# Optimization experiments

Hardware: AMD Instinct MI355X
Metric: run time of the kernel (lower is better)

Reference implementation:

```python
import jax, jax.numpy as jnp
import numpy as np

N_NODES = 100000


def _gcn_norm(edge_index, num_nodes):
    # PyG GCNConv default: add self-loops, symmetric normalization
    row, col = edge_index[0], edge_index[1]
    loop = jnp.arange(num_nodes, dtype=edge_index.dtype)
    row = jnp.concatenate([row, loop])
    col = jnp.concatenate([col, loop])
    ones = jnp.ones(col.shape[0], dtype=jnp.float32)
    deg = jax.ops.segment_sum(ones, col, num_segments=num_nodes)
    dinv = jnp.where(deg > 0, jax.lax.rsqrt(deg), 0.0)
    norm = dinv[row] * dinv[col]  # [E + N]
    return row, col, norm


def _gcn_conv(x, W, b, row, col, norm, num_nodes):
    h = x @ W                               # [N, out] linear transform first
    msg = h[row] * norm[:, None]            # gather + edge-wise scale
    out = jax.ops.segment_sum(msg, col, num_segments=num_nodes)  # scatter-add
    return out + b


def setup_inputs() -> dict:
    key = jax.random.key(0)
    k1, k2, k3, k4 = jax.random.split(key, 4)
    E = 1600000
    x = jax.random.normal(k1, (N_NODES, 128), dtype=jnp.float32)
    edge_index = jax.random.randint(k2, (2, E), 0, N_NODES, dtype=jnp.int64)
    W1 = jax.random.normal(k3, (128, 128), dtype=jnp.float32) * (1.0 / np.sqrt(128))
    b1 = jnp.zeros((128,), dtype=jnp.float32)
    W2 = jax.random.normal(k4, (128, 64), dtype=jnp.float32) * (1.0 / np.sqrt(128))
    b2 = jnp.zeros((64,), dtype=jnp.float32)
    return {"x": x, "edge_index": edge_index, "W1": W1, "b1": b1, "W2": W2, "b2": b2}


def reference(x, edge_index, W1, b1, W2, b2):
    num_nodes = x.shape[0]
    row, col, norm = _gcn_norm(edge_index, num_nodes)
    h = _gcn_conv(x, W1, b1, row, col, norm, num_nodes)
    h = jax.nn.relu(h)
    out = _gcn_conv(h, W2, b2, row, col, norm, num_nodes)
    return out
```

## Files before the change

kernel.cpp:

```cpp
#include <hip/hip_runtime.h>
#include <hip/hip_bf16.h>

typedef unsigned short u16;
typedef unsigned char u8;
typedef short bf16x8 __attribute__((ext_vector_type(8)));
typedef float f32x4 __attribute__((ext_vector_type(4)));

__device__ __forceinline__ float bflo(unsigned u) { return __uint_as_float(u << 16); }
__device__ __forceinline__ float bfhi(unsigned u) { return __uint_as_float(u & 0xffff0000u); }
__device__ __forceinline__ u16 f2bf(float f) {
    unsigned u = __float_as_uint(f);
    return (u16)((u + 0x7fffu + ((u >> 16) & 1u)) >> 16);
}

#define CHUNK 8192
#define BN 512

#define PK_RMASK 0x7fffffu

__global__ __launch_bounds__(256) void hist_prep_kernel(const int* __restrict__ cols,
                                                        unsigned* __restrict__ hist,
                                                        int E, int nbuckets, int nblocksA,
                                                        const float* __restrict__ W1,
                                                        const float* __restrict__ W2,
                                                        u16* __restrict__ WT1,
                                                        u16* __restrict__ WT2) {
    int blk = blockIdx.x;
    if (blk >= nblocksA) {
        int t = (blk - nblocksA) * 256 + threadIdx.x;
        if (t < 128 * 128) {
            int n = t >> 7, k = t & 127;
            WT1[n * 128 + k] = f2bf(W1[k * 128 + n]);
        } else if (t < 128 * 128 + 64 * 128) {
            int i = t - 128 * 128;
            int n = i >> 7, k = i & 127;
            WT2[n * 128 + k] = f2bf(W2[k * 64 + n]);
        }
        return;
    }
    __shared__ unsigned h[256];
    int t = threadIdx.x;
    h[t] = 0;
    __syncthreads();
    int base = blk * CHUNK;
#pragma unroll
    for (int j = 0; j < CHUNK / 256; j++) {
        int i = base + j * 256 + t;
        if (i < E) atomicAdd(&h[((unsigned)cols[i]) >> 9], 1u);
    }
    __syncthreads();
    if (t < nbuckets) hist[blk * nbuckets + t] = h[t];
}

__global__ __launch_bounds__(256) void scanA1_kernel(unsigned* __restrict__ hist,
                                                     unsigned* __restrict__ totals,
                                                     int nblocksA, int nbuckets) {
    __shared__ unsigned s[256];
    int t = threadIdx.x, b = blockIdx.x;
    unsigned val = (t < nblocksA) ? hist[t * nbuckets + b] : 0u;
    s[t] = val;
    __syncthreads();
    for (int off = 1; off < 256; off <<= 1) {
        unsigned v = (t >= off) ? s[t - off] : 0u;
        __syncthreads();
        s[t] += v;
        __syncthreads();
    }
    if (t < nblocksA) hist[t * nbuckets + b] = s[t] - val;
    if (t == 255) totals[b] = s[255];
}

__global__ __launch_bounds__(256) void scanA2_kernel(const unsigned* __restrict__ totals,
                                                     unsigned* __restrict__ bucketbase,
                                                     int nbuckets) {
    __shared__ unsigned s[256];
    int t = threadIdx.x;
    unsigned val = (t < nbuckets) ? totals[t] : 0u;
    s[t] = val;
    __syncthreads();
    for (int off = 1; off < 256; off <<= 1) {
        unsigned v = (t >= off) ? s[t - off] : 0u;
        __syncthreads();
        s[t] += v;
        __syncthreads();
    }
    unsigned ex = s[t] - val;
    if (t < nbuckets) bucketbase[t] = ex;
    if (t == nbuckets - 1) bucketbase[nbuckets] = ex + val;
}

__global__ __launch_bounds__(256) void scatterA_kernel(const int* __restrict__ rows,
                                                       const int* __restrict__ cols,
                                                       const unsigned* __restrict__ hist,
                                                       const unsigned* __restrict__ bucketbase,
                                                       unsigned* __restrict__ binned,
                                                       int E, int nbuckets) {
    __shared__ unsigned sp[CHUNK];
    __shared__ u8 spg[CHUNK];
    __shared__ unsigned lstart[256];
    __shared__ unsigned lcur[256];
    __shared__ unsigned gbase[256];
    int t = threadIdx.x, blk = blockIdx.x;
    int base = blk * CHUNK;
    int cnt = min(CHUNK, E - base);

    lcur[t] = 0;
    __syncthreads();
    for (int i = t; i < cnt; i += 256)
        atomicAdd(&lcur[((unsigned)cols[base + i]) >> 9], 1u);
    __syncthreads();
    unsigned val = lcur[t];
    lstart[t] = val;
    __syncthreads();
    for (int off = 1; off < 256; off <<= 1) {
        unsigned v = (t >= off) ? lstart[t - off] : 0u;
        __syncthreads();
        lstart[t] += v;
        __syncthreads();
    }
    unsigned ex = lstart[t] - val;
    __syncthreads();
    lstart[t] = ex;
    lcur[t] = ex;
    if (t < nbuckets) gbase[t] = bucketbase[t] + hist[blk * nbuckets + t];
    __syncthreads();
    for (int i = t; i < cnt; i += 256) {
        unsigned c = (unsigned)cols[base + i];
        unsigned r = (unsigned)rows[base + i];
        unsigned g = c >> 9;
        unsigned pos = atomicAdd(&lcur[g], 1u);
        sp[pos] = r | ((c & 511u) << 23);
        spg[pos] = (u8)g;
    }
    __syncthreads();
    for (int i = t; i < cnt; i += 256) {
        unsigned pk = sp[i];
        unsigned g = spg[i];
        binned[gbase[g] + (unsigned)i - lstart[g]] = pk;
    }
}

__global__ __launch_bounds__(256) void binB_kernel(const unsigned* __restrict__ binned,
                                                   const unsigned* __restrict__ bucketbase,
                                                   int* __restrict__ rowptr,
                                                   float* __restrict__ dinv,
                                                   int* __restrict__ srcidx,
                                                   int N, int E, int nbuckets) {
    __shared__ unsigned cnt[BN + 1];
    __shared__ unsigned sc[BN + 1];
    __shared__ unsigned ps[256];
    int t = threadIdx.x, b = blockIdx.x;
    int lo = b << 9;
    int nn = min(BN, N - lo);
    unsigned s = bucketbase[b], e = bucketbase[b + 1];

    cnt[t] = 0;
    cnt[t + 256] = 0;
    if (t == 0) cnt[BN] = 0;
    __syncthreads();
    for (unsigned i = s + t; i < e; i += 256)
        atomicAdd(&cnt[binned[i] >> 23], 1u);
    __syncthreads();

    unsigned a0 = cnt[2 * t], a1 = cnt[2 * t + 1];
    ps[t] = a0 + a1;
    __syncthreads();
    unsigned val = ps[t];
    for (int off = 1; off < 256; off <<= 1) {
        unsigned v = (t >= off) ? ps[t - off] : 0u;
        __syncthreads();
        ps[t] += v;
        __syncthreads();
    }
    unsigned ex = ps[t] - val;
    sc[2 * t] = ex;
    sc[2 * t + 1] = ex + a0;
    if (t == 255) sc[BN] = ex + val;
    __syncthreads();

    for (int n = t; n < nn; n += 256) {
        unsigned rp = s + sc[n];
        rowptr[lo + n] = (int)rp;
        dinv[lo + n] = rsqrtf((float)(sc[n + 1] - sc[n]) + 1.0f);
        cnt[n] = rp;
    }
    if (b == nbuckets - 1 && t == 0) rowptr[N] = E;
    __syncthreads();

    for (unsigned i = s + t; i < e; i += 256) {
        unsigned pk = binned[i];
        unsigned slot = atomicAdd(&cnt[pk >> 23], 1u);
        srcidx[slot] = (int)(pk & PK_RMASK);
    }
}

template <int NOUT, bool IN_BF16>
__global__ __launch_bounds__(256) void gemm_mfma(const void* __restrict__ Xv,
                                                 const u16* __restrict__ WT,
                                                 const float* __restrict__ dinv,
                                                 u16* __restrict__ OutH, int nrows) {
    constexpr int LDK = 136;
    __shared__ u16 sX[64 * LDK];
    __shared__ u16 sW[NOUT * LDK];

    const int t = threadIdx.x;
    const int wv = t >> 6, lane = t & 63;
    const int m = lane & 15, q = lane >> 4;
    const int row0 = blockIdx.x * 64;

    for (int idx = t; idx < NOUT * 16; idx += 256) {
        int n = idx >> 4, c = idx & 15;
        *((uint4*)&sW[n * LDK + c * 8]) = ((const uint4*)WT)[idx];
    }
    if (IN_BF16) {
        const u16* X = (const u16*)Xv;
        for (int idx = t; idx < 64 * 16; idx += 256) {
            int r = idx >> 4, c = idx & 15;
            int gr = row0 + r;
            uint4 v = make_uint4(0u, 0u, 0u, 0u);
            if (gr < nrows) v = ((const uint4*)X)[(size_t)gr * 16 + c];
            *((uint4*)&sX[r * LDK + c * 8]) = v;
        }
    } else {
        const float* X = (const float*)Xv;
        for (int idx = t; idx < 64 * 32; idx += 256) {
            int r = idx >> 5, c = idx & 31;
            int gr = row0 + r;
            float4 v = make_float4(0.f, 0.f, 0.f, 0.f);
            if (gr < nrows) v = ((const float4*)X)[(size_t)gr * 32 + c];
            uint2 o;
            o.x = (unsigned)f2bf(v.x) | ((unsigned)f2bf(v.y) << 16);
            o.y = (unsigned)f2bf(v.z) | ((unsigned)f2bf(v.w) << 16);
            *((uint2*)&sX[r * LDK + c * 4]) = o;
        }
    }
    __syncthreads();

    f32x4 acc[NOUT / 16];
#pragma unroll
    for (int i = 0; i < NOUT / 16; i++) acc[i] = (f32x4){0.f, 0.f, 0.f, 0.f};

#pragma unroll
    for (int ks = 0; ks < 4; ks++) {
        const int k0 = ks * 32 + q * 8;
        bf16x8 a = *((const bf16x8*)&sX[(wv * 16 + m) * LDK + k0]);
#pragma unroll
        for (int nt = 0; nt < NOUT / 16; nt++) {
            bf16x8 b = *((const bf16x8*)&sW[(nt * 16 + m) * LDK + k0]);
            acc[nt] = __builtin_amdgcn_mfma_f32_16x16x32_bf16(a, b, acc[nt], 0, 0, 0);
        }
    }

#pragma unroll
    for (int r = 0; r < 4; r++) {
        int gi = row0 + wv * 16 + q * 4 + r;
        if (gi < nrows) {
            float dv = dinv[gi];
#pragma unroll
            for (int nt = 0; nt < NOUT / 16; nt++) {
                OutH[(size_t)gi * NOUT + nt * 16 + m] = f2bf(acc[nt][r] * dv);
            }
        }
    }
}

__global__ __launch_bounds__(512) void agg1_gemm2(const int* __restrict__ rowptr,
                                                  const int* __restrict__ srcidx,
                                                  const u16* __restrict__ hs,
                                                  const float* __restrict__ dinv,
                                                  const float* __restrict__ bias,
                                                  const u16* __restrict__ WT2,
                                                  u16* __restrict__ h2s, int N) {
    constexpr int WPN = 16;
    constexpr int LDK = 136;
    constexpr int NPB = 32;
    __shared__ u16 sO[NPB * LDK];
    __shared__ u16 sW[64 * LDK];

    const int t = threadIdx.x;
    const int node_l = t / WPN;
    const int fl = t % WPN;
    const int node = blockIdx.x * NPB + node_l;
    const bool valid = node < N;

    for (int idx = t; idx < 64 * 16; idx += 512) {
        int n = idx >> 4, c = idx & 15;
        *((uint4*)&sW[n * LDK + c * 8]) = ((const uint4*)WT2)[idx];
    }

    const uint4* h128 = (const uint4*)hs;
    float a[8];
#pragma unroll
    for (int j = 0; j < 8; j++) a[j] = 0.f;

    if (valid) {
        int start = rowptr[node], end = rowptr[node + 1];
        {
            uint4 v = h128[(size_t)node * WPN + fl];
            a[0] = bflo(v.x); a[1] = bfhi(v.x); a[2] = bflo(v.y); a[3] = bfhi(v.y);
            a[4] = bflo(v.z); a[5] = bfhi(v.z); a[6] = bflo(v.w); a[7] = bfhi(v.w);
        }
        int nfull = (end - start) >> 3;
        int i = start;
        int r[8], r2[8];
        if (nfull > 0) {
#pragma unroll
            for (int j = 0; j < 8; j++) r[j] = srcidx[i + j];
        }
        for (int b = 0; b < nfull; b++) {
            uint4 u[8];
#pragma unroll
            for (int j = 0; j < 8; j++) u[j] = h128[(size_t)r[j] * WPN + fl];
            if (b + 1 < nfull) {
#pragma unroll
                for (int j = 0; j < 8; j++) r2[j] = srcidx[i + 8 + j];
            }
#pragma unroll
            for (int j = 0; j < 8; j++) {
                a[0] += bflo(u[j].x); a[1] += bfhi(u[j].x);
                a[2] += bflo(u[j].y); a[3] += bfhi(u[j].y);
                a[4] += bflo(u[j].z); a[5] += bfhi(u[j].z);
                a[6] += bflo(u[j].w); a[7] += bfhi(u[j].w);
            }
#pragma unroll
            for (int j = 0; j < 8; j++) r[j] = r2[j];
            i += 8;
        }
        if (i + 4 <= end) {
            int rr[4];
#pragma unroll
            for (int j = 0; j < 4; j++) rr[j] = srcidx[i + j];
            uint4 u[4];
#pragma unroll
            for (int j = 0; j < 4; j++) u[j] = h128[(size_t)rr[j] * WPN + fl];
#pragma unroll
            for (int j = 0; j < 4; j++) {
                a[0] += bflo(u[j].x); a[1] += bfhi(u[j].x);
                a[2] += bflo(u[j].y); a[3] += bfhi(u[j].y);
                a[4] += bflo(u[j].z); a[5] += bfhi(u[j].z);
                a[6] += bflo(u[j].w); a[7] += bfhi(u[j].w);
            }
            i += 4;
        }
        for (; i < end; ++i) {
            uint4 u = h128[(size_t)srcidx[i] * WPN + fl];
            a[0] += bflo(u.x); a[1] += bfhi(u.x);
            a[2] += bflo(u.y); a[3] += bfhi(u.y);
            a[4] += bflo(u.z); a[5] += bfhi(u.z);
            a[6] += bflo(u.w); a[7] += bfhi(u.w);
        }
    }

    float dv = valid ? dinv[node] : 0.f;
    float4 bv0 = ((const float4*)bias)[2 * fl];
    float4 bv1 = ((const float4*)bias)[2 * fl + 1];
    float o[8];
    o[0] = fmaxf(dv * a[0] + bv0.x, 0.f); o[1] = fmaxf(dv * a[1] + bv0.y, 0.f);
    o[2] = fmaxf(dv * a[2] + bv0.z, 0.f); o[3] = fmaxf(dv * a[3] + bv0.w, 0.f);
    o[4] = fmaxf(dv * a[4] + bv1.x, 0.f); o[5] = fmaxf(dv * a[5] + bv1.y, 0.f);
    o[6] = fmaxf(dv * a[6] + bv1.z, 0.f); o[7] = fmaxf(dv * a[7] + bv1.w, 0.f);
    uint4 w;
    w.x = (unsigned)f2bf(o[0]) | ((unsigned)f2bf(o[1]) << 16);
    w.y = (unsigned)f2bf(o[2]) | ((unsigned)f2bf(o[3]) << 16);
    w.z = (unsigned)f2bf(o[4]) | ((unsigned)f2bf(o[5]) << 16);
    w.w = (unsigned)f2bf(o[6]) | ((unsigned)f2bf(o[7]) << 16);
    *((uint4*)&sO[node_l * LDK + fl * 8]) = w;
    __syncthreads();

    const int wv = t >> 6, lane = t & 63;
    const int m = lane & 15, q = lane >> 4;
    const int nh = wv >> 2;
    const int ft = wv & 3;
    f32x4 acc = (f32x4){0.f, 0.f, 0.f, 0.f};
#pragma unroll
    for (int ks = 0; ks < 4; ks++) {
        const int k0 = ks * 32 + q * 8;
        bf16x8 af = *((const bf16x8*)&sO[(nh * 16 + m) * LDK + k0]);
        bf16x8 bf = *((const bf16x8*)&sW[(ft * 16 + m) * LDK + k0]);
        acc = __builtin_amdgcn_mfma_f32_16x16x32_bf16(af, bf, acc, 0, 0, 0);
    }
#pragma unroll
    for (int r = 0; r < 4; r++) {
        int gi = blockIdx.x * NPB + nh * 16 + q * 4 + r;
        if (gi < N) {
            float dvv = dinv[gi];
            h2s[(size_t)gi * 64 + ft * 16 + m] = f2bf(acc[r] * dvv);
        }
    }
}

template <int NH, bool RELU, bool OUT_BF16>
__global__ __launch_bounds__(256) void aggregate(const int* __restrict__ rowptr,
                                                 const int* __restrict__ srcidx,
                                                 const u16* __restrict__ hs,
                                                 const float* __restrict__ dinv,
                                                 const float* __restrict__ bias,
                                                 void* __restrict__ outv, int N) {
    constexpr int WPN = NH / 8;
    int tid = blockIdx.x * 256 + threadIdx.x;
    int node = tid / WPN;
    int fl = tid % WPN;
    if (node >= N) return;

    const uint4* h128 = (const uint4*)hs;
    int start = rowptr[node], end = rowptr[node + 1];

    float a[8];
    {
        uint4 v = h128[(size_t)node * WPN + fl];
        a[0] = bflo(v.x); a[1] = bfhi(v.x); a[2] = bflo(v.y); a[3] = bfhi(v.y);
        a[4] = bflo(v.z); a[5] = bfhi(v.z); a[6] = bflo(v.w); a[7] = bfhi(v.w);
    }

    int nfull = (end - start) >> 3;
    int i = start;
    int r[8], r2[8];
    if (nfull > 0) {
#pragma unroll
        for (int j = 0; j < 8; j++) r[j] = srcidx[i + j];
    }
    for (int b = 0; b < nfull; b++) {
        uint4 u[8];
#pragma unroll
        for (int j = 0; j < 8; j++) u[j] = h128[(size_t)r[j] * WPN + fl];
        if (b + 1 < nfull) {
#pragma unroll
            for (int j = 0; j < 8; j++) r2[j] = srcidx[i + 8 + j];
        }
#pragma unroll
        for (int j = 0; j < 8; j++) {
            a[0] += bflo(u[j].x); a[1] += bfhi(u[j].x);
            a[2] += bflo(u[j].y); a[3] += bfhi(u[j].y);
            a[4] += bflo(u[j].z); a[5] += bfhi(u[j].z);
            a[6] += bflo(u[j].w); a[7] += bfhi(u[j].w);
        }
#pragma unroll
        for (int j = 0; j < 8; j++) r[j] = r2[j];
        i += 8;
    }
    if (i + 4 <= end) {
        int rr[4];
#pragma unroll
        for (int j = 0; j < 4; j++) rr[j] = srcidx[i + j];
        uint4 u[4];
#pragma unroll
        for (int j = 0; j < 4; j++) u[j] = h128[(size_t)rr[j] * WPN + fl];
#pragma unroll
        for (int j = 0; j < 4; j++) {
            a[0] += bflo(u[j].x); a[1] += bfhi(u[j].x);
            a[2] += bflo(u[j].y); a[3] += bfhi(u[j].y);
            a[4] += bflo(u[j].z); a[5] += bfhi(u[j].z);
            a[6] += bflo(u[j].w); a[7] += bfhi(u[j].w);
        }
        i += 4;
    }
    for (; i < end; ++i) {
        uint4 u = h128[(size_t)srcidx[i] * WPN + fl];
        a[0] += bflo(u.x); a[1] += bfhi(u.x);
        a[2] += bflo(u.y); a[3] += bfhi(u.y);
        a[4] += bflo(u.z); a[5] += bfhi(u.z);
        a[6] += bflo(u.w); a[7] += bfhi(u.w);
    }

    float dv = dinv[node];
    float4 bv0 = ((const float4*)bias)[2 * fl];
    float4 bv1 = ((const float4*)bias)[2 * fl + 1];
    float o[8];
    o[0] = dv * a[0] + bv0.x; o[1] = dv * a[1] + bv0.y;
    o[2] = dv * a[2] + bv0.z; o[3] = dv * a[3] + bv0.w;
    o[4] = dv * a[4] + bv1.x; o[5] = dv * a[5] + bv1.y;
    o[6] = dv * a[6] + bv1.z; o[7] = dv * a[7] + bv1.w;
    if (RELU) {
#pragma unroll
        for (int j = 0; j < 8; j++) o[j] = fmaxf(o[j], 0.f);
    }
    if (OUT_BF16) {
        uint4 w;
        w.x = (unsigned)f2bf(o[0]) | ((unsigned)f2bf(o[1]) << 16);
        w.y = (unsigned)f2bf(o[2]) | ((unsigned)f2bf(o[3]) << 16);
        w.z = (unsigned)f2bf(o[4]) | ((unsigned)f2bf(o[5]) << 16);
        w.w = (unsigned)f2bf(o[6]) | ((unsigned)f2bf(o[7]) << 16);
        ((uint4*)outv)[tid] = w;
    } else {
        ((float4*)outv)[2 * tid] = make_float4(o[0], o[1], o[2], o[3]);
        ((float4*)outv)[2 * tid + 1] = make_float4(o[4], o[5], o[6], o[7]);
    }
}

extern "C" void kernel_launch(void* const* d_in, const int* in_sizes, int n_in,
                              void* d_out, int out_size, void* d_ws, size_t ws_size,
                              hipStream_t stream) {
    const float* x  = (const float*)d_in[0];
    const int*   ei = (const int*)d_in[1];
    const float* W1 = (const float*)d_in[2];
    const float* b1 = (const float*)d_in[3];
    const float* W2 = (const float*)d_in[4];
    const float* b2 = (const float*)d_in[5];

    const int N = in_sizes[0] / 128;
    const int E = in_sizes[1] / 2;
    const int* rows = ei;
    const int* cols = ei + E;

    const int nbuckets = (N + BN - 1) / BN;
    const int nblocksA = (E + CHUNK - 1) / CHUNK;

    char* ws = (char*)d_ws;
    size_t off = 0;
    auto alloc = [&](size_t bytes) -> void* {
        void* p = ws + off;
        off = (off + bytes + 1023) & ~(size_t)1023;
        return p;
    };
    unsigned* hist       = (unsigned*)alloc((size_t)nbuckets * nblocksA * 4);
    unsigned* totals     = (unsigned*)alloc(256 * 4);
    unsigned* bucketbase = (unsigned*)alloc((size_t)(nbuckets + 1) * 4);
    unsigned* binned     = (unsigned*)alloc((size_t)E * 4);
    int*      rowptr     = (int*)alloc((size_t)(N + 1) * 4);
    float*    dinv       = (float*)alloc((size_t)N * 4);
    int*      srcidx     = (int*)alloc((size_t)E * 4);
    u16*      WT1        = (u16*)alloc((size_t)128 * 128 * 2);
    u16*      WT2        = (u16*)alloc((size_t)64 * 128 * 2);
    u16*      h1s        = (u16*)alloc((size_t)N * 128 * 2);
    u16*      h2s        = (u16*)alloc((size_t)N * 64 * 2);

    hist_prep_kernel<<<nblocksA + 96, 256, 0, stream>>>(cols, hist, E, nbuckets, nblocksA,
                                                        W1, W2, WT1, WT2);
    scanA1_kernel<<<nbuckets, 256, 0, stream>>>(hist, totals, nblocksA, nbuckets);
    scanA2_kernel<<<1, 256, 0, stream>>>(totals, bucketbase, nbuckets);
    scatterA_kernel<<<nblocksA, 256, 0, stream>>>(rows, cols, hist, bucketbase, binned, E, nbuckets);
    binB_kernel<<<nbuckets, 256, 0, stream>>>(binned, bucketbase, rowptr, dinv, srcidx, N, E, nbuckets);

    gemm_mfma<128, false><<<(N + 63) / 64, 256, 0, stream>>>(x, WT1, dinv, h1s, N);

    agg1_gemm2<<<(N + 31) / 32, 512, 0, stream>>>(rowptr, srcidx, h1s, dinv, b1, WT2, h2s, N);

    aggregate<64, false, false><<<(N * 8 + 255) / 256, 256, 0, stream>>>(
        rowptr, srcidx, h2s, dinv, b2, d_out, N);
}
```

Baseline: 276.6 us.

## Fuse bucket scan kernels via last-block pattern and shrink agg1_gemm2 blocks

Merges the two scan kernels into one, using an atomic completion counter so the last block to finish computes the bucket-base prefix over the totals. This removes one kernel launch. The agg1_gemm2 kernel now uses 256-thread blocks that each handle 16 nodes. It drops the shared-memory staging of WT2 and reads the B fragments straight from global memory, which lowers LDS use and should raise occupancy, at the cost of repeated global or L2 reads of WT2.

```diff
diff --git a/kernel.cpp b/kernel.cpp
--- a/kernel.cpp
+++ b/kernel.cpp
@@ -24,8 +24,10 @@
                                                         const float* __restrict__ W1,
                                                         const float* __restrict__ W2,
                                                         u16* __restrict__ WT1,
-                                                        u16* __restrict__ WT2) {
+                                                        u16* __restrict__ WT2,
+                                                        unsigned* __restrict__ done) {
     int blk = blockIdx.x;
+    if (blk == 0 && threadIdx.x == 0) *done = 0u;
     if (blk >= nblocksA) {
         int t = (blk - nblocksA) * 256 + threadIdx.x;
         if (t < 128 * 128) {
@@ -52,10 +54,13 @@
     if (t < nbuckets) hist[blk * nbuckets + t] = h[t];
 }
 
-__global__ __launch_bounds__(256) void scanA1_kernel(unsigned* __restrict__ hist,
-                                                     unsigned* __restrict__ totals,
-                                                     int nblocksA, int nbuckets) {
+__global__ __launch_bounds__(256) void scanA_fused(unsigned* __restrict__ hist,
+                                                   unsigned* __restrict__ totals,
+                                                   unsigned* __restrict__ bucketbase,
+                                                   unsigned* __restrict__ done,
+                                                   int nblocksA, int nbuckets) {
     __shared__ unsigned s[256];
+    __shared__ unsigned rank;
     int t = threadIdx.x, b = blockIdx.x;
     unsigned val = (t < nblocksA) ? hist[t * nbuckets + b] : 0u;
     s[t] = val;
@@ -68,15 +73,13 @@
     }
     if (t < nblocksA) hist[t * nbuckets + b] = s[t] - val;
     if (t == 255) totals[b] = s[255];
-}
-
-__global__ __launch_bounds__(256) void scanA2_kernel(const unsigned* __restrict__ totals,
-                                                     unsigned* __restrict__ bucketbase,
-                                                     int nbuckets) {
-    __shared__ unsigned s[256];
-    int t = threadIdx.x;
-    unsigned val = (t < nbuckets) ? totals[t] : 0u;
-    s[t] = val;
+    __threadfence();
+    if (t == 0) rank = atomicAdd(done, 1u);
+    __syncthreads();
+    if (rank != (unsigned)(gridDim.x - 1)) return;
+
+    unsigned tv = (t < nbuckets) ? atomicAdd(&totals[t], 0u) : 0u;
+    s[t] = tv;
     __syncthreads();
     for (int off = 1; off < 256; off <<= 1) {
         unsigned v = (t >= off) ? s[t - off] : 0u;
@@ -84,9 +87,9 @@
         s[t] += v;
         __syncthreads();
     }
-    unsigned ex = s[t] - val;
+    unsigned ex = s[t] - tv;
     if (t < nbuckets) bucketbase[t] = ex;
-    if (t == nbuckets - 1) bucketbase[nbuckets] = ex + val;
+    if (t == nbuckets - 1) bucketbase[nbuckets] = ex + tv;
 }
 
 __global__ __launch_bounds__(256) void scatterA_kernel(const int* __restrict__ rows,
@@ -264,7 +267,7 @@
     }
 }
 
-__global__ __launch_bounds__(512) void agg1_gemm2(const int* __restrict__ rowptr,
+__global__ __launch_bounds__(256) void agg1_gemm2(const int* __restrict__ rowptr,
                                                   const int* __restrict__ srcidx,
                                                   const u16* __restrict__ hs,
                                                   const float* __restrict__ dinv,
@@ -273,20 +276,13 @@
                                                   u16* __restrict__ h2s, int N) {
     constexpr int WPN = 16;
     constexpr int LDK = 136;
-    constexpr int NPB = 32;
-    __shared__ u16 sO[NPB * LDK];
-    __shared__ u16 sW[64 * LDK];
+    __shared__ u16 sO[16 * LDK];
 
     const int t = threadIdx.x;
     const int node_l = t / WPN;
     const int fl = t % WPN;
-    const int node = blockIdx.x * NPB + node_l;
+    const int node = blockIdx.x * 16 + node_l;
     const bool valid = node < N;
-
-    for (int idx = t; idx < 64 * 16; idx += 512) {
-        int n = idx >> 4, c = idx & 15;
-        *((uint4*)&sW[n * LDK + c * 8]) = ((const uint4*)WT2)[idx];
-    }
 
     const uint4* h128 = (const uint4*)hs;
     float a[8];
@@ -369,22 +365,20 @@
 
     const int wv = t >> 6, lane = t & 63;
     const int m = lane & 15, q = lane >> 4;
-    const int nh = wv >> 2;
-    const int ft = wv & 3;
     f32x4 acc = (f32x4){0.f, 0.f, 0.f, 0.f};
 #pragma unroll
     for (int ks = 0; ks < 4; ks++) {
         const int k0 = ks * 32 + q * 8;
-        bf16x8 af = *((const bf16x8*)&sO[(nh * 16 + m) * LDK + k0]);
-        bf16x8 bf = *((const bf16x8*)&sW[(ft * 16 + m) * LDK + k0]);
+        bf16x8 af = *((const bf16x8*)&sO[m * LDK + k0]);
+        bf16x8 bf = *((const bf16x8*)&WT2[(wv * 16 + m) * 128 + k0]);
         acc = __builtin_amdgcn_mfma_f32_16x16x32_bf16(af, bf, acc, 0, 0, 0);
     }
 #pragma unroll
     for (int r = 0; r < 4; r++) {
-        int gi = blockIdx.x * NPB + nh * 16 + q * 4 + r;
+        int gi = blockIdx.x * 16 + q * 4 + r;
         if (gi < N) {
             float dvv = dinv[gi];
-            h2s[(size_t)gi * 64 + ft * 16 + m] = f2bf(acc[r] * dvv);
+            h2s[(size_t)gi * 64 + wv * 16 + m] = f2bf(acc[r] * dvv);
         }
     }
 }
@@ -515,6 +509,7 @@
     unsigned* hist       = (unsigned*)alloc((size_t)nbuckets * nblocksA * 4);
     unsigned* totals     = (unsigned*)alloc(256 * 4);
     unsigned* bucketbase = (unsigned*)alloc((size_t)(nbuckets + 1) * 4);
+    unsigned* done       = (unsigned*)alloc(4);
     unsigned* binned     = (unsigned*)alloc((size_t)E * 4);
     int*      rowptr     = (int*)alloc((size_t)(N + 1) * 4);
     float*    dinv       = (float*)alloc((size_t)N * 4);
@@ -525,15 +520,14 @@
     u16*      h2s        = (u16*)alloc((size_t)N * 64 * 2);
 
     hist_prep_kernel<<<nblocksA + 96, 256, 0, stream>>>(cols, hist, E, nbuckets, nblocksA,
-                                                        W1, W2, WT1, WT2);
-    scanA1_kernel<<<nbuckets, 256, 0, stream>>>(hist, totals, nblocksA, nbuckets);
-    scanA2_kernel<<<1, 256, 0, stream>>>(totals, bucketbase, nbuckets);
+                                                        W1, W2, WT1, WT2, done);
+    scanA_fused<<<nbuckets, 256, 0, stream>>>(hist, totals, bucketbase, done, nblocksA, nbuckets);
     scatterA_kernel<<<nblocksA, 256, 0, stream>>>(rows, cols, hist, bucketbase, binned, E, nbuckets);
     binB_kernel<<<nbuckets, 256, 0, stream>>>(binned, bucketbase, rowptr, dinv, srcidx, N, E, nbuckets);
 
     gemm_mfma<128, false><<<(N + 63) / 64, 256, 0, stream>>>(x, WT1, dinv, h1s, N);
 
-    agg1_gemm2<<<(N + 31) / 32, 512, 0, stream>>>(rowptr, srcidx, h1s, dinv, b1, WT2, h2s, N);
+    agg1_gemm2<<<(N + 15) / 16, 256, 0, stream>>>(rowptr, srcidx, h1s, dinv, b1, WT2, h2s, N);
 
     aggregate<64, false, false><<<(N * 8 + 255) / 256, 256, 0, stream>>>(
         rowptr, srcidx, h2s, dinv, b2, d_out, N);
```

Result: slower. 286.7 us (+3.6%).

## Sort nodes by degree within buckets to balance aggregation wavefronts

Applied to the files above, without the earlier changes.

binB now builds, for each 512-node bucket, a permutation that orders nodes by in-degree (capped at 63) using a shared-memory counting sort. The aggregation kernels visit nodes through this permutation, so nodes with similar degree share a wavefront and lanes diverge less in their neighbour loops. agg1_gemm2 is also shrunk to 16 nodes and 256 threads per block, and its MFMA is remapped so each wave computes one 16-column tile of the output. The cost is an extra indirection through perm, scattered output writes, and loading the W2 tile into shared memory twice as many times in total.

```diff
diff --git a/kernel.cpp b/kernel.cpp
--- a/kernel.cpp
+++ b/kernel.cpp
@@ -145,10 +145,13 @@
                                                    int* __restrict__ rowptr,
                                                    float* __restrict__ dinv,
                                                    int* __restrict__ srcidx,
+                                                   int* __restrict__ perm,
                                                    int N, int E, int nbuckets) {
     __shared__ unsigned cnt[BN + 1];
     __shared__ unsigned sc[BN + 1];
     __shared__ unsigned ps[256];
+    __shared__ unsigned dh[64];
+    __shared__ unsigned dcur[64];
     int t = threadIdx.x, b = blockIdx.x;
     int lo = b << 9;
     int nn = min(BN, N - lo);
@@ -186,6 +189,26 @@
     }
     if (b == nbuckets - 1 && t == 0) rowptr[N] = E;
     __syncthreads();
+
+    if (t < 64) dh[t] = 0;
+    __syncthreads();
+    for (int n = t; n < nn; n += 256) {
+        unsigned d = min(sc[n + 1] - sc[n], 63u);
+        atomicAdd(&dh[d], 1u);
+    }
+    __syncthreads();
+    if (t == 0) {
+        unsigned acc = 0;
+        for (int d = 0; d < 64; d++) { unsigned c = dh[d]; dh[d] = acc; acc += c; }
+    }
+    __syncthreads();
+    if (t < 64) dcur[t] = dh[t];
+    __syncthreads();
+    for (int n = t; n < nn; n += 256) {
+        unsigned d = min(sc[n + 1] - sc[n], 63u);
+        unsigned p = atomicAdd(&dcur[d], 1u);
+        perm[lo + (int)p] = lo + n;
+    }
 
     for (unsigned i = s + t; i < e; i += 256) {
         unsigned pk = binned[i];
@@ -264,28 +287,29 @@
     }
 }
 
-__global__ __launch_bounds__(512) void agg1_gemm2(const int* __restrict__ rowptr,
+__global__ __launch_bounds__(256) void agg1_gemm2(const int* __restrict__ rowptr,
                                                   const int* __restrict__ srcidx,
                                                   const u16* __restrict__ hs,
                                                   const float* __restrict__ dinv,
                                                   const float* __restrict__ bias,
                                                   const u16* __restrict__ WT2,
+                                                  const int* __restrict__ perm,
                                                   u16* __restrict__ h2s, int N) {
     constexpr int WPN = 16;
     constexpr int LDK = 136;
-    constexpr int NPB = 32;
-    __shared__ u16 sO[NPB * LDK];
+    __shared__ u16 sO[16 * LDK];
     __shared__ u16 sW[64 * LDK];
 
     const int t = threadIdx.x;
     const int node_l = t / WPN;
     const int fl = t % WPN;
-    const int node = blockIdx.x * NPB + node_l;
-    const bool valid = node < N;
-
-    for (int idx = t; idx < 64 * 16; idx += 512) {
-        int n = idx >> 4, c = idx & 15;
-        *((uint4*)&sW[n * LDK + c * 8]) = ((const uint4*)WT2)[idx];
+    const int idx = blockIdx.x * 16 + node_l;
+    const bool valid = idx < N;
+    const int node = valid ? perm[idx] : 0;
+
+    for (int i2 = t; i2 < 64 * 16; i2 += 256) {
+        int n = i2 >> 4, c = i2 & 15;
+        *((uint4*)&sW[n * LDK + c * 8]) = ((const uint4*)WT2)[i2];
     }
 
     const uint4* h128 = (const uint4*)hs;
@@ -369,22 +393,21 @@
 
     const int wv = t >> 6, lane = t & 63;
     const int m = lane & 15, q = lane >> 4;
-    const int nh = wv >> 2;
-    const int ft = wv & 3;
     f32x4 acc = (f32x4){0.f, 0.f, 0.f, 0.f};
 #pragma unroll
     for (int ks = 0; ks < 4; ks++) {
         const int k0 = ks * 32 + q * 8;
-        bf16x8 af = *((const bf16x8*)&sO[(nh * 16 + m) * LDK + k0]);
-        bf16x8 bf = *((const bf16x8*)&sW[(ft * 16 + m) * LDK + k0]);
+        bf16x8 af = *((const bf16x8*)&sO[m * LDK + k0]);
+        bf16x8 bf = *((const bf16x8*)&sW[(wv * 16 + m) * LDK + k0]);
         acc = __builtin_amdgcn_mfma_f32_16x16x32_bf16(af, bf, acc, 0, 0, 0);
     }
 #pragma unroll
     for (int r = 0; r < 4; r++) {
-        int gi = blockIdx.x * NPB + nh * 16 + q * 4 + r;
-        if (gi < N) {
-            float dvv = dinv[gi];
-            h2s[(size_t)gi * 64 + ft * 16 + m] = f2bf(acc[r] * dvv);
+        int gidx = blockIdx.x * 16 + q * 4 + r;
+        if (gidx < N) {
+            int gnode = perm[gidx];
+            float dvv = dinv[gnode];
+            h2s[(size_t)gnode * 64 + wv * 16 + m] = f2bf(acc[r] * dvv);
         }
     }
 }
@@ -395,12 +418,14 @@
                                                  const u16* __restrict__ hs,
                                                  const float* __restrict__ dinv,
                                                  const float* __restrict__ bias,
+                                                 const int* __restrict__ perm,
                                                  void* __restrict__ outv, int N) {
     constexpr int WPN = NH / 8;
     int tid = blockIdx.x * 256 + threadIdx.x;
-    int node = tid / WPN;
+    int idx = tid / WPN;
     int fl = tid % WPN;
-    if (node >= N) return;
+    if (idx >= N) return;
+    int node = perm[idx];
 
     const uint4* h128 = (const uint4*)hs;
     int start = rowptr[node], end = rowptr[node + 1];
@@ -474,16 +499,17 @@
 #pragma unroll
         for (int j = 0; j < 8; j++) o[j] = fmaxf(o[j], 0.f);
     }
+    size_t obase = (size_t)node * WPN + fl;
     if (OUT_BF16) {
         uint4 w;
         w.x = (unsigned)f2bf(o[0]) | ((unsigned)f2bf(o[1]) << 16);
         w.y = (unsigned)f2bf(o[2]) | ((unsigned)f2bf(o[3]) << 16);
         w.z = (unsigned)f2bf(o[4]) | ((unsigned)f2bf(o[5]) << 16);
         w.w = (unsigned)f2bf(o[6]) | ((unsigned)f2bf(o[7]) << 16);
-        ((uint4*)outv)[tid] = w;
+        ((uint4*)outv)[obase] = w;
     } else {
-        ((float4*)outv)[2 * tid] = make_float4(o[0], o[1], o[2], o[3]);
-        ((float4*)outv)[2 * tid + 1] = make_float4(o[4], o[5], o[6], o[7]);
+        ((float4*)outv)[2 * obase] = make_float4(o[0], o[1], o[2], o[3]);
+        ((float4*)outv)[2 * obase + 1] = make_float4(o[4], o[5], o[6], o[7]);
     }
 }
 
@@ -519,6 +545,7 @@
     int*      rowptr     = (int*)alloc((size_t)(N + 1) * 4);
     float*    dinv       = (float*)alloc((size_t)N * 4);
     int*      srcidx     = (int*)alloc((size_t)E * 4);
+    int*      perm       = (int*)alloc((size_t)N * 4);
     u16*      WT1        = (u16*)alloc((size_t)128 * 128 * 2);
     u16*      WT2        = (u16*)alloc((size_t)64 * 128 * 2);
     u16*      h1s        = (u16*)alloc((size_t)N * 128 * 2);
@@ -529,12 +556,13 @@
     scanA1_kernel<<<nbuckets, 256, 0, stream>>>(hist, totals, nblocksA, nbuckets);
     scanA2_kernel<<<1, 256, 0, stream>>>(totals, bucketbase, nbuckets);
     scatterA_kernel<<<nblocksA, 256, 0, stream>>>(rows, cols, hist, bucketbase, binned, E, nbuckets);
-    binB_kernel<<<nbuckets, 256, 0, stream>>>(binned, bucketbase, rowptr, dinv, srcidx, N, E, nbuckets);
+    binB_kernel<<<nbuckets, 256, 0, stream>>>(binned, bucketbase, rowptr, dinv, srcidx, perm,
+                                              N, E, nbuckets);
 
     gemm_mfma<128, false><<<(N + 63) / 64, 256, 0, stream>>>(x, WT1, dinv, h1s, N);
 
-    agg1_gemm2<<<(N + 31) / 32, 512, 0, stream>>>(rowptr, srcidx, h1s, dinv, b1, WT2, h2s, N);
+    agg1_gemm2<<<(N + 15) / 16, 256, 0, stream>>>(rowptr, srcidx, h1s, dinv, b1, WT2, perm, h2s, N);
 
     aggregate<64, false, false><<<(N * 8 + 255) / 256, 256, 0, stream>>>(
-        rowptr, srcidx, h2s, dinv, b2, d_out, N);
-}
+        rowptr, srcidx, h2s, dinv, b2, perm, d_out, N);
+}
```

After: 284.7 us. +2.9%, slower.

## Shrink binning chunks and halve fused agg1/GEMM2 block size

Applied to the files above, without the earlier changes.

The edge-binning chunk size drops from 8192 to 2048, so the histogram and scatter kernels launch more blocks. The per-bucket scan now handles up to 1024 blocks by having each thread sum four entries before the block scan. The fused layer-1 aggregation and layer-2 GEMM kernel moves from 512-thread blocks of 32 nodes to 256-thread blocks of 16 nodes, with each wave computing one 16-column tile. The aim is more parallelism and occupancy in the preprocessing and aggregation stages, at the cost of reloading W2 into shared memory more often and writing a larger histogram.

```diff
diff --git a/kernel.cpp b/kernel.cpp
--- a/kernel.cpp
+++ b/kernel.cpp
@@ -13,7 +13,7 @@
     return (u16)((u + 0x7fffu + ((u >> 16) & 1u)) >> 16);
 }
 
-#define CHUNK 8192
+#define CHUNK 2048
 #define BN 512
 
 #define PK_RMASK 0x7fffffu
@@ -57,16 +57,30 @@
                                                      int nblocksA, int nbuckets) {
     __shared__ unsigned s[256];
     int t = threadIdx.x, b = blockIdx.x;
-    unsigned val = (t < nblocksA) ? hist[t * nbuckets + b] : 0u;
-    s[t] = val;
-    __syncthreads();
+    unsigned v[4];
+    unsigned sum = 0;
+#pragma unroll
+    for (int k = 0; k < 4; k++) {
+        int blk = t * 4 + k;
+        v[k] = (blk < nblocksA) ? hist[(size_t)blk * nbuckets + b] : 0u;
+        sum += v[k];
+    }
+    s[t] = sum;
+    __syncthreads();
+    unsigned val = sum;
     for (int off = 1; off < 256; off <<= 1) {
-        unsigned v = (t >= off) ? s[t - off] : 0u;
-        __syncthreads();
-        s[t] += v;
-        __syncthreads();
-    }
-    if (t < nblocksA) hist[t * nbuckets + b] = s[t] - val;
+        unsigned x = (t >= off) ? s[t - off] : 0u;
+        __syncthreads();
+        s[t] += x;
+        __syncthreads();
+    }
+    unsigned ex = s[t] - val;
+#pragma unroll
+    for (int k = 0; k < 4; k++) {
+        int blk = t * 4 + k;
+        if (blk < nblocksA) hist[(size_t)blk * nbuckets + b] = ex;
+        ex += v[k];
+    }
     if (t == 255) totals[b] = s[255];
 }
 
@@ -122,7 +136,7 @@
     __syncthreads();
     lstart[t] = ex;
     lcur[t] = ex;
-    if (t < nbuckets) gbase[t] = bucketbase[t] + hist[blk * nbuckets + t];
+    if (t < nbuckets) gbase[t] = bucketbase[t] + hist[(size_t)blk * nbuckets + t];
     __syncthreads();
     for (int i = t; i < cnt; i += 256) {
         unsigned c = (unsigned)cols[base + i];
@@ -264,7 +278,7 @@
     }
 }
 
-__global__ __launch_bounds__(512) void agg1_gemm2(const int* __restrict__ rowptr,
+__global__ __launch_bounds__(256) void agg1_gemm2(const int* __restrict__ rowptr,
                                                   const int* __restrict__ srcidx,
                                                   const u16* __restrict__ hs,
                                                   const float* __restrict__ dinv,
@@ -273,17 +287,16 @@
                                                   u16* __restrict__ h2s, int N) {
     constexpr int WPN = 16;
     constexpr int LDK = 136;
-    constexpr int NPB = 32;
-    __shared__ u16 sO[NPB * LDK];
+    __shared__ u16 sO[16 * LDK];
     __shared__ u16 sW[64 * LDK];
 
     const int t = threadIdx.x;
     const int node_l = t / WPN;
     const int fl = t % WPN;
-    const int node = blockIdx.x * NPB + node_l;
+    const int node = blockIdx.x * 16 + node_l;
     const bool valid = node < N;
 
-    for (int idx = t; idx < 64 * 16; idx += 512) {
+    for (int idx = t; idx < 64 * 16; idx += 256) {
         int n = idx >> 4, c = idx & 15;
         *((uint4*)&sW[n * LDK + c * 8]) = ((const uint4*)WT2)[idx];
     }
@@ -369,22 +382,20 @@
 
     const int wv = t >> 6, lane = t & 63;
     const int m = lane & 15, q = lane >> 4;
-    const int nh = wv >> 2;
-    const int ft = wv & 3;
     f32x4 acc = (f32x4){0.f, 0.f, 0.f, 0.f};
 #pragma unroll
     for (int ks = 0; ks < 4; ks++) {
         const int k0 = ks * 32 + q * 8;
-        bf16x8 af = *((const bf16x8*)&sO[(nh * 16 + m) * LDK + k0]);
-        bf16x8 bf = *((const bf16x8*)&sW[(ft * 16 + m) * LDK + k0]);
+        bf16x8 af = *((const bf16x8*)&sO[m * LDK + k0]);
+        bf16x8 bf = *((const bf16x8*)&sW[(wv * 16 + m) * LDK + k0]);
         acc = __builtin_amdgcn_mfma_f32_16x16x32_bf16(af, bf, acc, 0, 0, 0);
     }
 #pragma unroll
     for (int r = 0; r < 4; r++) {
-        int gi = blockIdx.x * NPB + nh * 16 + q * 4 + r;
+        int gi = blockIdx.x * 16 + q * 4 + r;
         if (gi < N) {
             float dvv = dinv[gi];
-            h2s[(size_t)gi * 64 + ft * 16 + m] = f2bf(acc[r] * dvv);
+            h2s[(size_t)gi * 64 + wv * 16 + m] = f2bf(acc[r] * dvv);
         }
     }
 }
@@ -533,7 +544,7 @@
 
     gemm_mfma<128, false><<<(N + 63) / 64, 256, 0, stream>>>(x, WT1, dinv, h1s, N);
 
-    agg1_gemm2<<<(N + 31) / 32, 512, 0, stream>>>(rowptr, srcidx, h1s, dinv, b1, WT2, h2s, N);
+    agg1_gemm2<<<(N + 15) / 16, 256, 0, stream>>>(rowptr, srcidx, h1s, dinv, b1, WT2, h2s, N);
 
     aggregate<64, false, false><<<(N * 8 + 255) / 256, 256, 0, stream>>>(
         rowptr, srcidx, h2s, dinv, b2, d_out, N);
```

Result: faster. 261.4 us (median of 2 runs) (-5.5%).
